# Performance work log

Hardware: AMD Instinct MI355X
Metric: run time of the kernel (lower is better)

The kernel has to match this reference:

```python
import jax, jax.numpy as jnp
import numpy as np

CHANNELS = [4096, 4096, 4096, 4096]
SPARSITY = 0.9  # fraction of weight entries zeroed (sten.random_mask_sparsify frac)
BATCH = 4096


def _sparse_weight(key, out_f, in_f, frac):
    kw, km = jax.random.split(key)
    w = jax.random.normal(kw, (out_f, in_f), dtype=jnp.float32)
    keep = jax.random.uniform(km, (out_f, in_f)) >= frac  # keep ~(1-frac) entries
    return jnp.where(keep, w, 0.0)


def setup_inputs() -> dict:
    key = jax.random.key(0)
    ks = jax.random.split(key, 7)
    x = jax.random.normal(ks[0], (BATCH, CHANNELS[0]), dtype=jnp.float32)
    W1 = _sparse_weight(ks[1], CHANNELS[1], CHANNELS[0], SPARSITY)
    b1 = jax.random.uniform(ks[2], (CHANNELS[1],), dtype=jnp.float32)
    W2 = _sparse_weight(ks[3], CHANNELS[2], CHANNELS[1], SPARSITY)
    b2 = jax.random.uniform(ks[4], (CHANNELS[2],), dtype=jnp.float32)
    W3 = _sparse_weight(ks[5], CHANNELS[3], CHANNELS[2], SPARSITY)
    b3 = jax.random.uniform(ks[6], (CHANNELS[3],), dtype=jnp.float32)
    return {"x": x, "W1": W1, "b1": b1, "W2": W2, "b2": b2, "W3": W3, "b3": b3}


def reference(x, W1, b1, W2, b2, W3, b3):
    # Sequential: Linear -> ReLU -> Linear -> ReLU -> Linear
    # F.linear(x, W, b) == x @ W.T + b; weights already carry the sparsity mask.
    h = x @ W1.T + b1
    h = jax.nn.relu(h)
    h = h @ W2.T + b2
    h = jax.nn.relu(h)
    return h @ W3.T + b3
```

## Files before the change

kernel.cpp:

```cpp
#include <hip/hip_runtime.h>
#include <cstdint>


#define MATN 4096

typedef _Float16 half8 __attribute__((ext_vector_type(8)));
typedef float f32x4 __attribute__((ext_vector_type(4)));

__device__ __forceinline__ void glds16(const void* g, void* l) {
    __builtin_amdgcn_global_load_lds(
        (const __attribute__((address_space(1))) char*)(uintptr_t)g,
        (__attribute__((address_space(3))) char*)(uintptr_t)l,
        16, 0, 0);
}

__device__ __forceinline__ void cvt_body(const float* __restrict__ in,
                                         _Float16* __restrict__ out, int n8) {
    for (int g = blockIdx.x * 256 + threadIdx.x; g < n8; g += gridDim.x * 256) {
        size_t i = (size_t)g * 8;
        float4 a = *(const float4*)(in + i);
        float4 b = *(const float4*)(in + i + 4);
        half8 o;
        o[0] = (_Float16)a.x; o[1] = (_Float16)a.y;
        o[2] = (_Float16)a.z; o[3] = (_Float16)a.w;
        o[4] = (_Float16)b.x; o[5] = (_Float16)b.y;
        o[6] = (_Float16)b.z; o[7] = (_Float16)b.w;
        *(half8*)(out + i) = o;
    }
}

__global__ __launch_bounds__(256)
void cvt_f16(const float* __restrict__ in, _Float16* __restrict__ out, int n8) {
    cvt_body(in, out, n8);
}

__global__ __launch_bounds__(256)
void cvt_f16_2(const float* __restrict__ i0, _Float16* __restrict__ o0,
               const float* __restrict__ i1, _Float16* __restrict__ o1, int n8) {
    cvt_body(blockIdx.y ? i1 : i0, blockIdx.y ? o1 : o0, n8);
}

template <bool RELU, typename OutT>
__global__ __launch_bounds__(256, 4)
void gemm_bt(const _Float16* __restrict__ A, const _Float16* __restrict__ B,
             const float* __restrict__ bias, OutT* __restrict__ C) {
    __shared__ _Float16 sA[128 * 64];
    __shared__ _Float16 sB[128 * 64];

    const int tid  = threadIdx.x;
    const int lane = tid & 63;
    const int w    = tid >> 6;
    const int wm   = w >> 1;
    const int wn   = w & 1;
    const int l16  = lane & 15;
    const int kq   = lane >> 4;

    const int tileM = blockIdx.y * 128;
    const int tileN = blockIdx.x * 128;

    f32x4 acc[4][4] = {};

    const int rin = tid >> 3;
    const int gch = (tid & 7) ^ (rin & 7);
    const _Float16* Ap = A + (size_t)(tileM + rin) * MATN + gch * 8;
    const _Float16* Bp = B + (size_t)(tileN + rin) * MATN + gch * 8;
    const size_t rstep = (size_t)32 * MATN;

    char* sAl = (char*)sA + w * 1024;
    char* sBl = (char*)sB + w * 1024;

    const int sl0 = kq ^ (l16 & 7);
    const int sl1 = sl0 ^ 4;
    const _Float16* rA0 = sA + (wm * 64 + l16) * 64 + sl0 * 8;
    const _Float16* rA1 = sA + (wm * 64 + l16) * 64 + sl1 * 8;
    const _Float16* rB0 = sB + (wn * 64 + l16) * 64 + sl0 * 8;
    const _Float16* rB1 = sB + (wn * 64 + l16) * 64 + sl1 * 8;

    for (int k0 = 0; k0 < MATN; k0 += 64) {
#pragma unroll
        for (int c = 0; c < 4; ++c) glds16(Ap + c * rstep, sAl + c * 4096);
#pragma unroll
        for (int c = 0; c < 4; ++c) glds16(Bp + c * rstep, sBl + c * 4096);
        Ap += 64; Bp += 64;
        __syncthreads();

        half8 af[4], bf[4];
#pragma unroll
        for (int mi = 0; mi < 4; ++mi) af[mi] = *(const half8*)(rA0 + mi * 1024);
#pragma unroll
        for (int ni = 0; ni < 4; ++ni) bf[ni] = *(const half8*)(rB0 + ni * 1024);
#pragma unroll
        for (int mi = 0; mi < 4; ++mi)
#pragma unroll
            for (int ni = 0; ni < 4; ++ni)
                acc[mi][ni] = __builtin_amdgcn_mfma_f32_16x16x32_f16(
                    af[mi], bf[ni], acc[mi][ni], 0, 0, 0);
#pragma unroll
        for (int mi = 0; mi < 4; ++mi) af[mi] = *(const half8*)(rA1 + mi * 1024);
#pragma unroll
        for (int ni = 0; ni < 4; ++ni) bf[ni] = *(const half8*)(rB1 + ni * 1024);
#pragma unroll
        for (int mi = 0; mi < 4; ++mi)
#pragma unroll
            for (int ni = 0; ni < 4; ++ni)
                acc[mi][ni] = __builtin_amdgcn_mfma_f32_16x16x32_f16(
                    af[mi], bf[ni], acc[mi][ni], 0, 0, 0);
        __syncthreads();
    }

#pragma unroll
    for (int ni = 0; ni < 4; ++ni) {
        const int gn = tileN + wn * 64 + ni * 16 + l16;
        const float bv = bias[gn];
#pragma unroll
        for (int mi = 0; mi < 4; ++mi) {
            const int gm = tileM + wm * 64 + mi * 16 + kq * 4;
#pragma unroll
            for (int r = 0; r < 4; ++r) {
                float v = acc[mi][ni][r] + bv;
                if (RELU) v = v > 0.f ? v : 0.f;
                C[(size_t)(gm + r) * MATN + gn] = (OutT)v;
            }
        }
    }
}

extern "C" void kernel_launch(void* const* d_in, const int* in_sizes, int n_in,
                              void* d_out, int out_size, void* d_ws, size_t ws_size,
                              hipStream_t stream) {
    const float* x  = (const float*)d_in[0];
    const float* W1 = (const float*)d_in[1];
    const float* b1 = (const float*)d_in[2];
    const float* W2 = (const float*)d_in[3];
    const float* b2 = (const float*)d_in[4];
    const float* W3 = (const float*)d_in[5];
    const float* b3 = (const float*)d_in[6];
    float* out = (float*)d_out;

    const size_t MAT = (size_t)MATN * MATN;
    _Float16* xb = (_Float16*)d_ws;
    _Float16* wb = (_Float16*)((char*)d_ws + MAT * 2);
    _Float16* h1 = (_Float16*)((char*)d_ws + MAT * 4);
    _Float16* h2 = xb;

    const int n8 = (int)(MAT / 8);
    dim3 ggrid(MATN / 128, MATN / 128);

    cvt_f16_2<<<dim3(2048, 2), 256, 0, stream>>>(x, xb, W1, wb, n8);
    gemm_bt<true, _Float16><<<ggrid, 256, 0, stream>>>(xb, wb, b1, h1);

    cvt_f16<<<2048, 256, 0, stream>>>(W2, wb, n8);
    gemm_bt<true, _Float16><<<ggrid, 256, 0, stream>>>(h1, wb, b2, h2);

    cvt_f16<<<2048, 256, 0, stream>>>(W3, wb, n8);
    gemm_bt<false, float><<<ggrid, 256, 0, stream>>>(h2, wb, b3, out);
}
```

Baseline: 594.3 us.

## Widen GEMM tiles to 128x256, swizzle block order, batch all conversions

Each GEMM block now computes a 128x256 output tile with 4x8 MFMA accumulators per wave and loads a larger B tile into shared memory. Occupancy is lowered to 3 blocks per CU to make room for the extra registers. Block IDs are remapped so that blocks running at the same time share tiles in L2. When the workspace is large enough, all four fp32->fp16 conversions run in one launch into separate buffers, which cuts the number of kernel launches. The cost is higher register and LDS pressure, a grid of 512 blocks that may leave CUs unevenly loaded, and a larger workspace requirement.

```diff
diff --git a/kernel.cpp b/kernel.cpp
--- a/kernel.cpp
+++ b/kernel.cpp
@@ -40,12 +40,30 @@
     cvt_body(blockIdx.y ? i1 : i0, blockIdx.y ? o1 : o0, n8);
 }
 
+__global__ __launch_bounds__(256)
+void cvt_f16_4(const float* __restrict__ i0, _Float16* __restrict__ o0,
+               const float* __restrict__ i1, _Float16* __restrict__ o1,
+               const float* __restrict__ i2, _Float16* __restrict__ o2,
+               const float* __restrict__ i3, _Float16* __restrict__ o3, int n8) {
+    const float* in;
+    _Float16* out;
+    switch (blockIdx.y) {
+        case 0: in = i0; out = o0; break;
+        case 1: in = i1; out = o1; break;
+        case 2: in = i2; out = o2; break;
+        default: in = i3; out = o3; break;
+    }
+    cvt_body(in, out, n8);
+}
+
+#define MFMA_(d, x, y) d = __builtin_amdgcn_mfma_f32_16x16x32_f16(x, y, d, 0, 0, 0)
+
 template <bool RELU, typename OutT>
-__global__ __launch_bounds__(256, 4)
+__global__ __launch_bounds__(256, 3)
 void gemm_bt(const _Float16* __restrict__ A, const _Float16* __restrict__ B,
              const float* __restrict__ bias, OutT* __restrict__ C) {
     __shared__ _Float16 sA[128 * 64];
-    __shared__ _Float16 sB[128 * 64];
+    __shared__ _Float16 sB[256 * 64];
 
     const int tid  = threadIdx.x;
     const int lane = tid & 63;
@@ -55,10 +73,12 @@
     const int l16  = lane & 15;
     const int kq   = lane >> 4;
 
-    const int tileM = blockIdx.y * 128;
-    const int tileN = blockIdx.x * 128;
+    const int bid   = blockIdx.y * 16 + blockIdx.x;
+    const int sbid  = (bid & 7) * 64 + (bid >> 3);
+    const int tileM = (sbid >> 4) * 128;
+    const int tileN = (sbid & 15) * 256;
 
-    f32x4 acc[4][4] = {};
+    f32x4 acc[4][8] = {};
 
     const int rin = tid >> 3;
     const int gch = (tid & 7) ^ (rin & 7);
@@ -73,44 +93,40 @@
     const int sl1 = sl0 ^ 4;
     const _Float16* rA0 = sA + (wm * 64 + l16) * 64 + sl0 * 8;
     const _Float16* rA1 = sA + (wm * 64 + l16) * 64 + sl1 * 8;
-    const _Float16* rB0 = sB + (wn * 64 + l16) * 64 + sl0 * 8;
-    const _Float16* rB1 = sB + (wn * 64 + l16) * 64 + sl1 * 8;
+    const _Float16* rB0 = sB + (wn * 128 + l16) * 64 + sl0 * 8;
+    const _Float16* rB1 = sB + (wn * 128 + l16) * 64 + sl1 * 8;
 
     for (int k0 = 0; k0 < MATN; k0 += 64) {
 #pragma unroll
         for (int c = 0; c < 4; ++c) glds16(Ap + c * rstep, sAl + c * 4096);
 #pragma unroll
-        for (int c = 0; c < 4; ++c) glds16(Bp + c * rstep, sBl + c * 4096);
+        for (int c = 0; c < 8; ++c) glds16(Bp + c * rstep, sBl + c * 4096);
         Ap += 64; Bp += 64;
         __syncthreads();
 
-        half8 af[4], bf[4];
+        half8 a[4], b[8];
 #pragma unroll
-        for (int mi = 0; mi < 4; ++mi) af[mi] = *(const half8*)(rA0 + mi * 1024);
+        for (int mi = 0; mi < 4; ++mi) a[mi] = *(const half8*)(rA0 + mi * 1024);
 #pragma unroll
-        for (int ni = 0; ni < 4; ++ni) bf[ni] = *(const half8*)(rB0 + ni * 1024);
+        for (int ni = 0; ni < 8; ++ni) b[ni] = *(const half8*)(rB0 + ni * 1024);
 #pragma unroll
         for (int mi = 0; mi < 4; ++mi)
 #pragma unroll
-            for (int ni = 0; ni < 4; ++ni)
-                acc[mi][ni] = __builtin_amdgcn_mfma_f32_16x16x32_f16(
-                    af[mi], bf[ni], acc[mi][ni], 0, 0, 0);
+            for (int ni = 0; ni < 8; ++ni) MFMA_(acc[mi][ni], a[mi], b[ni]);
 #pragma unroll
-        for (int mi = 0; mi < 4; ++mi) af[mi] = *(const half8*)(rA1 + mi * 1024);
+        for (int mi = 0; mi < 4; ++mi) a[mi] = *(const half8*)(rA1 + mi * 1024);
 #pragma unroll
-        for (int ni = 0; ni < 4; ++ni) bf[ni] = *(const half8*)(rB1 + ni * 1024);
+        for (int ni = 0; ni < 8; ++ni) b[ni] = *(const half8*)(rB1 + ni * 1024);
 #pragma unroll
         for (int mi = 0; mi < 4; ++mi)
 #pragma unroll
-            for (int ni = 0; ni < 4; ++ni)
-                acc[mi][ni] = __builtin_amdgcn_mfma_f32_16x16x32_f16(
-                    af[mi], bf[ni], acc[mi][ni], 0, 0, 0);
+            for (int ni = 0; ni < 8; ++ni) MFMA_(acc[mi][ni], a[mi], b[ni]);
         __syncthreads();
     }
 
 #pragma unroll
-    for (int ni = 0; ni < 4; ++ni) {
-        const int gn = tileN + wn * 64 + ni * 16 + l16;
+    for (int ni = 0; ni < 8; ++ni) {
+        const int gn = tileN + wn * 128 + ni * 16 + l16;
         const float bv = bias[gn];
 #pragma unroll
         for (int mi = 0; mi < 4; ++mi) {
@@ -138,20 +154,34 @@
     float* out = (float*)d_out;
 
     const size_t MAT = (size_t)MATN * MATN;
-    _Float16* xb = (_Float16*)d_ws;
-    _Float16* wb = (_Float16*)((char*)d_ws + MAT * 2);
-    _Float16* h1 = (_Float16*)((char*)d_ws + MAT * 4);
-    _Float16* h2 = xb;
+    const size_t HB  = MAT * 2;
+    const int n8 = (int)(MAT / 8);
+    dim3 ggrid(MATN / 256, MATN / 128);
 
-    const int n8 = (int)(MAT / 8);
-    dim3 ggrid(MATN / 128, MATN / 128);
+    if (ws_size >= HB * 5) {
+        _Float16* xb = (_Float16*)d_ws;
+        _Float16* w1 = (_Float16*)((char*)d_ws + HB);
+        _Float16* w2 = (_Float16*)((char*)d_ws + HB * 2);
+        _Float16* w3 = (_Float16*)((char*)d_ws + HB * 3);
+        _Float16* h1 = (_Float16*)((char*)d_ws + HB * 4);
+        _Float16* h2 = xb;
 
-    cvt_f16_2<<<dim3(2048, 2), 256, 0, stream>>>(x, xb, W1, wb, n8);
-    gemm_bt<true, _Float16><<<ggrid, 256, 0, stream>>>(xb, wb, b1, h1);
+        cvt_f16_4<<<dim3(2048, 4), 256, 0, stream>>>(x, xb, W1, w1, W2, w2,
+                                                     W3, w3, n8);
+        gemm_bt<true, _Float16><<<ggrid, 256, 0, stream>>>(xb, w1, b1, h1);
+        gemm_bt<true, _Float16><<<ggrid, 256, 0, stream>>>(h1, w2, b2, h2);
+        gemm_bt<false, float><<<ggrid, 256, 0, stream>>>(h2, w3, b3, out);
+    } else {
+        _Float16* xb = (_Float16*)d_ws;
+        _Float16* wb = (_Float16*)((char*)d_ws + HB);
+        _Float16* h1 = (_Float16*)((char*)d_ws + HB * 2);
+        _Float16* h2 = xb;
 
-    cvt_f16<<<2048, 256, 0, stream>>>(W2, wb, n8);
-    gemm_bt<true, _Float16><<<ggrid, 256, 0, stream>>>(h1, wb, b2, h2);
-
-    cvt_f16<<<2048, 256, 0, stream>>>(W3, wb, n8);
-    gemm_bt<false, float><<<ggrid, 256, 0, stream>>>(h2, wb, b3, out);
+        cvt_f16_2<<<dim3(2048, 2), 256, 0, stream>>>(x, xb, W1, wb, n8);
+        gemm_bt<true, _Float16><<<ggrid, 256, 0, stream>>>(xb, wb, b1, h1);
+        cvt_f16<<<2048, 256, 0, stream>>>(W2, wb, n8);
+        gemm_bt<true, _Float16><<<ggrid, 256, 0, stream>>>(h1, wb, b2, h2);
+        cvt_f16<<<2048, 256, 0, stream>>>(W3, wb, n8);
+        gemm_bt<false, float><<<ggrid, 256, 0, stream>>>(h2, wb, b3, out);
+    }
 }
```

Measured after the change: 963.5 us. +62.1%, slower.
